# Optimization experiments

Measured on AMD Instinct MI355X. Metric: run time of the kernel, lower is better.

The kernel has to match this reference:

```python
import jax, jax.numpy as jnp
import numpy as np

SEQLS = [256, 256, 256, 256]
HEADS = 8
DIM_HEAD = 64
DIM = 512
SCALE = DIM_HEAD ** -0.5
EPS = 1e-5
# static segment-id per token position: [N]
SEG = np.repeat(np.arange(len(SEQLS)), SEQLS)


def setup_inputs() -> dict:
    key = jax.random.key(0)
    k_x, k_m, k_qkv, k_out = jax.random.split(key, 4)
    B, N = 8, sum(SEQLS)
    inner = HEADS * DIM_HEAD
    x = jax.random.normal(k_x, (B, N, DIM), dtype=jnp.float32)
    m_labels = jax.random.randint(k_m, (B, len(SEQLS)), 0, 2)
    gamma = jnp.ones((DIM,), jnp.float32)
    beta = jnp.zeros((DIM,), jnp.float32)
    w_qkv = jax.random.normal(k_qkv, (DIM, 3 * inner), jnp.float32) * (DIM ** -0.5)
    w_out = jax.random.normal(k_out, (inner, DIM), jnp.float32) * (inner ** -0.5)
    b_out = jnp.zeros((DIM,), jnp.float32)
    return {"x": x, "m_labels": m_labels, "gamma": gamma, "beta": beta,
            "w_qkv": w_qkv, "w_out": w_out, "b_out": b_out}


def reference(x, m_labels, gamma, beta, w_qkv, w_out, b_out):
    B, N, _ = x.shape
    # LayerNorm
    mu = jnp.mean(x, axis=-1, keepdims=True)
    var = jnp.var(x, axis=-1, keepdims=True)
    h = (x - mu) * jax.lax.rsqrt(var + EPS) * gamma + beta
    # QKV projection (no bias)
    qkv = h @ w_qkv  # [B, N, 3*inner]
    q, k, v = jnp.split(qkv, 3, axis=-1)
    to_heads = lambda t: t.reshape(B, N, HEADS, DIM_HEAD).transpose(0, 2, 1, 3)
    q, k, v = to_heads(q), to_heads(k), to_heads(v)  # [B, H, N, D]
    dots = jnp.einsum('bhid,bhjd->bhij', q, k) * SCALE  # [B, H, N, N]
    # modality-block additive mask: -inf on any row/col of a missing modality
    missing = (m_labels == 0)[:, SEG]  # [B, N]
    blocked = missing[:, :, None] | missing[:, None, :]  # [B, N, N]
    dots = jnp.where(blocked[:, None, :, :], -jnp.inf, dots)
    # custom softmax: rows that are fully -inf output 0
    all_inf = jnp.all(jnp.isinf(dots), axis=-1, keepdims=True)
    safe = jnp.where(all_inf, 0.0, dots)
    attn = jax.nn.softmax(safe, axis=-1)
    attn = jnp.where(all_inf, 0.0, attn)
    out = jnp.einsum('bhij,bhjd->bhid', attn, v)  # [B, H, N, D]
    out = out.transpose(0, 2, 1, 3).reshape(B, N, HEADS * DIM_HEAD)
    return out @ w_out + b_out
```

## Files before the change

kernel.cpp:

```cpp
#include <hip/hip_runtime.h>

typedef _Float16 f16;
typedef _Float16 f16x8 __attribute__((ext_vector_type(8)));
typedef float f32x4 __attribute__((ext_vector_type(4)));

typedef __attribute__((address_space(1))) void gvoid;
typedef __attribute__((address_space(3))) void lvoid;
#define GLD16(gp, lp) __builtin_amdgcn_global_load_lds((gvoid*)(gp), (lvoid*)(lp), 16, 0, 0)

__device__ __forceinline__ f32x4 mfma16(f16x8 a, f16x8 b, f32x4 c) {
    return __builtin_amdgcn_mfma_f32_16x16x32_f16(a, b, c, 0, 0, 0);
}

__global__ __launch_bounds__(256) void k_prep(
    const float* __restrict__ x, const float* __restrict__ gamma,
    const float* __restrict__ beta, const int* __restrict__ mlab,
    const float* __restrict__ wqkv, const float* __restrict__ wout,
    f16* __restrict__ h, f16* __restrict__ wqkvT, f16* __restrict__ woutT)
{
    __shared__ float t[64][65];
    int bid = blockIdx.x, tid = threadIdx.x;
    if (bid < 2048) {
        int row = bid * 4 + (tid >> 6);
        int b = row >> 10, seg = (row >> 8) & 3;
        if (mlab[b * 4 + seg] == 0) return;
        int lane = tid & 63;
        const float* xr = x + (size_t)row * 512;
        float4 a = ((const float4*)xr)[lane * 2];
        float4 bv = ((const float4*)xr)[lane * 2 + 1];
        float v[8] = {a.x, a.y, a.z, a.w, bv.x, bv.y, bv.z, bv.w};
        float s = 0.f, s2 = 0.f;
#pragma unroll
        for (int j = 0; j < 8; ++j) { s += v[j]; s2 += v[j] * v[j]; }
#pragma unroll
        for (int off = 1; off < 64; off <<= 1) {
            s  += __shfl_xor(s, off);
            s2 += __shfl_xor(s2, off);
        }
        float mu  = s * (1.f / 512.f);
        float var = s2 * (1.f / 512.f) - mu * mu;
        float rstd = rsqrtf(var + 1e-5f);
        float4 g0 = ((const float4*)gamma)[lane * 2];
        float4 g1 = ((const float4*)gamma)[lane * 2 + 1];
        float4 b0 = ((const float4*)beta)[lane * 2];
        float4 b1 = ((const float4*)beta)[lane * 2 + 1];
        float g[8]  = {g0.x, g0.y, g0.z, g0.w, g1.x, g1.y, g1.z, g1.w};
        float bb[8] = {b0.x, b0.y, b0.z, b0.w, b1.x, b1.y, b1.z, b1.w};
        f16x8 o;
#pragma unroll
        for (int j = 0; j < 8; ++j) o[j] = (f16)((v[j] - mu) * rstd * g[j] + bb[j]);
        *(f16x8*)&h[(size_t)row * 512 + lane * 8] = o;
        return;
    }
    const float* in; f16* out; int C, c0, r0;
    if (bid < 2240) { int idx = bid - 2048; in = wqkv; out = wqkvT; C = 1536; c0 = (idx % 24) * 64; r0 = (idx / 24) * 64; }
    else            { int idx = bid - 2240; in = wout; out = woutT; C = 512;  c0 = (idx % 8)  * 64; r0 = (idx / 8)  * 64; }
#pragma unroll
    for (int i = 0; i < 16; ++i) {
        int r = i * 4 + (tid >> 6), c = tid & 63;
        t[r][c] = in[(size_t)(r0 + r) * C + c0 + c];
    }
    __syncthreads();
#pragma unroll
    for (int i = 0; i < 16; ++i) {
        int cr = i * 4 + (tid >> 6), cc = tid & 63;
        out[(size_t)(c0 + cr) * 512 + r0 + cc] = (f16)t[cc][cr];
    }
}

__global__ __launch_bounds__(256, 3) void k_gemm_qkv(
    const f16* __restrict__ A, const f16* __restrict__ Bt, const int* __restrict__ mlab,
    f16* __restrict__ q, f16* __restrict__ kmat, f16* __restrict__ vt)
{
    __shared__ f16 As[2][64 * 64];
    __shared__ f16 Bs[2][128 * 64];
    int tid = threadIdx.x, wid = tid >> 6, lane = tid & 63;
    int wm = wid >> 1, wn = wid & 1;
    int l15 = lane & 15, l4 = lane >> 4;
    int rowBase = blockIdx.y * 64;
    int colBase = blockIdx.x * 128;
    if (mlab[(rowBase >> 10) * 4 + ((rowBase & 1023) >> 8)] == 0) return;

    int srow = lane >> 3;
    int scolz = ((lane & 7) ^ srow) << 3;
    int kxor = (l15 & 7) << 3;

#define STG(bi, kt)                                                                         \
    do {                                                                                    \
        _Pragma("unroll") for (int i_ = 0; i_ < 2; ++i_) {                                  \
            int rg = (wid * 2 + i_) * 8;                                                    \
            GLD16(&A[(size_t)(rowBase + rg + srow) * 512 + (kt) + scolz], &As[bi][rg * 64]);\
        }                                                                                   \
        _Pragma("unroll") for (int i_ = 0; i_ < 4; ++i_) {                                  \
            int rg = (wid * 4 + i_) * 8;                                                    \
            GLD16(&Bt[(size_t)(colBase + rg + srow) * 512 + (kt) + scolz], &Bs[bi][rg * 64]);\
        }                                                                                   \
    } while (0)

    f32x4 acc[2][4] = {};
    STG(0, 0);
    for (int ki = 0; ki < 8; ++ki) {
        int bi = ki & 1;
        __syncthreads();
        if (ki < 7) STG(bi ^ 1, (ki + 1) * 64);
#pragma unroll
        for (int kk = 0; kk < 2; ++kk) {
            f16x8 af[2], bf[4];
#pragma unroll
            for (int m = 0; m < 2; ++m)
                af[m] = *(const f16x8*)&As[bi][(wm * 32 + m * 16 + l15) * 64 + ((kk * 32 + l4 * 8) ^ kxor)];
#pragma unroll
            for (int n = 0; n < 4; ++n)
                bf[n] = *(const f16x8*)&Bs[bi][(wn * 64 + n * 16 + l15) * 64 + ((kk * 32 + l4 * 8) ^ kxor)];
#pragma unroll
            for (int m = 0; m < 2; ++m)
#pragma unroll
                for (int n = 0; n < 4; ++n)
                    acc[m][n] = mfma16(af[m], bf[n], acc[m][n]);
        }
    }
#undef STG
#pragma unroll
    for (int m = 0; m < 2; ++m)
#pragma unroll
        for (int n = 0; n < 4; ++n)
#pragma unroll
            for (int r = 0; r < 4; ++r) {
                int row = rowBase + wm * 32 + m * 16 + l4 * 4 + r;
                int col = colBase + wn * 64 + n * 16 + l15;
                f16 hv = (f16)acc[m][n][r];
                int b = row >> 10, nt = row & 1023;
                int which = col >> 9, hh = (col >> 6) & 7, d = col & 63;
                size_t hidx = ((size_t)(b * 8 + hh) * 1024 + nt) * 64 + d;
                if (which == 0)      q[hidx] = hv;
                else if (which == 1) kmat[hidx] = hv;
                else                 vt[((size_t)(b * 8 + hh) * 64 + d) * 1024 + nt] = hv;
            }
}

__global__ __launch_bounds__(256, 5) void k_attn(
    const f16* __restrict__ q, const f16* __restrict__ kmat,
    const f16* __restrict__ vt, const int* __restrict__ mlab,
    f16* __restrict__ ao)
{
    __shared__ f16 Ks[2][64 * 64];
    __shared__ f16 Vs[2][64 * 64];

    int bid = blockIdx.x;
    int bh = (bid & 7) + 8 * (bid >> 7);
    int qb = (bid >> 3) & 15;
    int b = bh >> 3, hh = bh & 7;
    int tid = threadIdx.x, wid = tid >> 6, lane = tid & 63;
    int l15 = lane & 15, l4 = lane >> 4;
    int qbase = qb * 64;
    size_t bhs = (size_t)bh;

    if (mlab[b * 4 + (qb >> 2)] == 0) return;

    unsigned long long chpack = 0; int nch = 0;
#pragma unroll
    for (int s = 0; s < 4; ++s)
        if (mlab[b * 4 + s] != 0) {
#pragma unroll
            for (int j = 0; j < 4; ++j) {
                chpack |= (unsigned long long)(4 * s + j) << (4 * nch);
                ++nch;
            }
        }

    f16x8 qf[2];
#pragma unroll
    for (int kk = 0; kk < 2; ++kk) {
        qf[kk] = *(const f16x8*)&q[(bhs * 1024 + qbase + wid * 16 + l15) * 64 + kk * 32 + l4 * 8];
#pragma unroll
        for (int j = 0; j < 8; ++j) qf[kk][j] = qf[kk][j] * (f16)0.125;
    }

    int srow0 = tid >> 3;
    int sc0 = ((tid & 7) ^ (srow0 & 7)) << 3;
    int srow1 = (tid + 256) >> 3;
    int sc1 = (((tid + 256) & 7) ^ (srow1 & 7)) << 3;
    int ldsbase0 = (wid * 64) * 8;
    int ldsbase1 = (wid * 64 + 256) * 8;

#define STAGE(bi, t0)                                                                   \
    do {                                                                                \
        GLD16(&kmat[(bhs * 1024 + (t0) + srow0) * 64 + sc0], &Ks[bi][ldsbase0]);        \
        GLD16(&kmat[(bhs * 1024 + (t0) + srow1) * 64 + sc1], &Ks[bi][ldsbase1]);        \
        GLD16(&vt[(bhs * 64 + srow0) * 1024 + (t0) + sc0],   &Vs[bi][ldsbase0]);        \
        GLD16(&vt[(bhs * 64 + srow1) * 1024 + (t0) + sc1],   &Vs[bi][ldsbase1]);        \
    } while (0)

    float mrun = -1e30f, lrun = 0.f;
    f32x4 o[4] = {};
    int kxor = (l15 & 7) << 3;
    int srcA = l15 + ((l4 & 1) * 2) * 16;
    int srcB = srcA + 16;
    int sel = l4 >> 1;

    STAGE(0, (int)(chpack & 15) << 6);

    for (int c = 0; c < nch; ++c) {
        int bi = c & 1;
        __syncthreads();
        if (c + 1 < nch) {
            int t0n = (int)((chpack >> (4 * (c + 1))) & 15) << 6;
            STAGE(bi ^ 1, t0n);
        }

        f32x4 st[4] = {};
#pragma unroll
        for (int kk = 0; kk < 2; ++kk)
#pragma unroll
            for (int n = 0; n < 4; ++n) {
                f16x8 ka = *(const f16x8*)&Ks[bi][(n * 16 + l15) * 64 + ((kk * 32 + l4 * 8) ^ kxor)];
                st[n] = mfma16(ka, qf[kk], st[n]);
            }

        f32x4 m4 = st[0];
#pragma unroll
        for (int n = 1; n < 4; ++n)
#pragma unroll
            for (int r = 0; r < 4; ++r) m4[r] = fmaxf(m4[r], st[n][r]);
        float mx = fmaxf(fmaxf(m4[0], m4[1]), fmaxf(m4[2], m4[3]));
        mx = fmaxf(mx, __shfl_xor(mx, 16));
        mx = fmaxf(mx, __shfl_xor(mx, 32));
        float mnew = fmaxf(mrun, mx);
        float alpha = __expf(mrun - mnew);
        mrun = mnew;
        float rs = 0.f;
        union PK { f16 h[4]; long long ll; } pk[4];
#pragma unroll
        for (int n = 0; n < 4; ++n)
#pragma unroll
            for (int r = 0; r < 4; ++r) {
                float p = __expf(st[n][r] - mnew);
                rs += p;
                pk[n].h[r] = (f16)p;
            }
        rs += __shfl_xor(rs, 16);
        rs += __shfl_xor(rs, 32);
        lrun = lrun * alpha + rs;
#pragma unroll
        for (int nd = 0; nd < 4; ++nd) o[nd] *= alpha;

#pragma unroll
        for (int ks = 0; ks < 2; ++ks) {
            long long A0 = __shfl(pk[ks * 2].ll,     srcA);
            long long A1 = __shfl(pk[ks * 2 + 1].ll, srcA);
            long long B0 = __shfl(pk[ks * 2].ll,     srcB);
            long long B1 = __shfl(pk[ks * 2 + 1].ll, srcB);
            union PB { long long ll[2]; f16x8 v; } pb;
            pb.ll[0] = sel ? A1 : A0;
            pb.ll[1] = sel ? B1 : B0;
#pragma unroll
            for (int nd = 0; nd < 4; ++nd) {
                f16x8 va = *(const f16x8*)&Vs[bi][(nd * 16 + l15) * 64 + ((ks * 32 + l4 * 8) ^ kxor)];
                o[nd] = mfma16(va, pb.v, o[nd]);
            }
        }
    }
#undef STAGE

    float inv = 1.f / lrun;
    int qrow = qbase + wid * 16 + l15;
#pragma unroll
    for (int nd = 0; nd < 4; ++nd) {
        union { f16 h[4]; long long ll; } w;
#pragma unroll
        for (int r = 0; r < 4; ++r) w.h[r] = (f16)(o[nd][r] * inv);
        *(long long*)&ao[(size_t)(b * 1024 + qrow) * 512 + hh * 64 + nd * 16 + l4 * 4] = w.ll;
    }
}

__global__ __launch_bounds__(256, 3) void k_gemm_out(
    const f16* __restrict__ A, const f16* __restrict__ Bt, const int* __restrict__ mlab,
    const float* __restrict__ bias, float* __restrict__ out)
{
    __shared__ f16 As[2][64 * 64];
    __shared__ f16 Bs[2][128 * 64];
    int tid = threadIdx.x, wid = tid >> 6, lane = tid & 63;
    int wm = wid >> 1, wn = wid & 1;
    int l15 = lane & 15, l4 = lane >> 4;
    int rowBase = blockIdx.y * 64;
    int colBase = blockIdx.x * 128;
    if (mlab[(rowBase >> 10) * 4 + ((rowBase & 1023) >> 8)] == 0) {
        for (int i = tid; i < 64 * 128; i += 256)
            out[(size_t)(rowBase + (i >> 7)) * 512 + colBase + (i & 127)] = bias[colBase + (i & 127)];
        return;
    }

    int srow = lane >> 3;
    int scolz = ((lane & 7) ^ srow) << 3;
    int kxor = (l15 & 7) << 3;

#define STG(bi, kt)                                                                         \
    do {                                                                                    \
        _Pragma("unroll") for (int i_ = 0; i_ < 2; ++i_) {                                  \
            int rg = (wid * 2 + i_) * 8;                                                    \
            GLD16(&A[(size_t)(rowBase + rg + srow) * 512 + (kt) + scolz], &As[bi][rg * 64]);\
        }                                                                                   \
        _Pragma("unroll") for (int i_ = 0; i_ < 4; ++i_) {                                  \
            int rg = (wid * 4 + i_) * 8;                                                    \
            GLD16(&Bt[(size_t)(colBase + rg + srow) * 512 + (kt) + scolz], &Bs[bi][rg * 64]);\
        }                                                                                   \
    } while (0)

    f32x4 acc[2][4] = {};
    STG(0, 0);
    for (int ki = 0; ki < 8; ++ki) {
        int bi = ki & 1;
        __syncthreads();
        if (ki < 7) STG(bi ^ 1, (ki + 1) * 64);
#pragma unroll
        for (int kk = 0; kk < 2; ++kk) {
            f16x8 af[2], bf[4];
#pragma unroll
            for (int m = 0; m < 2; ++m)
                af[m] = *(const f16x8*)&As[bi][(wm * 32 + m * 16 + l15) * 64 + ((kk * 32 + l4 * 8) ^ kxor)];
#pragma unroll
            for (int n = 0; n < 4; ++n)
                bf[n] = *(const f16x8*)&Bs[bi][(wn * 64 + n * 16 + l15) * 64 + ((kk * 32 + l4 * 8) ^ kxor)];
#pragma unroll
            for (int m = 0; m < 2; ++m)
#pragma unroll
                for (int n = 0; n < 4; ++n)
                    acc[m][n] = mfma16(af[m], bf[n], acc[m][n]);
        }
    }
#undef STG
#pragma unroll
    for (int m = 0; m < 2; ++m)
#pragma unroll
        for (int n = 0; n < 4; ++n)
#pragma unroll
            for (int r = 0; r < 4; ++r) {
                int row = rowBase + wm * 32 + m * 16 + l4 * 4 + r;
                int col = colBase + wn * 64 + n * 16 + l15;
                out[(size_t)row * 512 + col] = acc[m][n][r] + bias[col];
            }
}

extern "C" void kernel_launch(void* const* d_in, const int* in_sizes, int n_in,
                              void* d_out, int out_size, void* d_ws, size_t ws_size,
                              hipStream_t stream) {
    const float* x     = (const float*)d_in[0];
    const int*   mlab  = (const int*)d_in[1];
    const float* gamma = (const float*)d_in[2];
    const float* beta  = (const float*)d_in[3];
    const float* wqkv  = (const float*)d_in[4];
    const float* wout  = (const float*)d_in[5];
    const float* bout  = (const float*)d_in[6];
    float* out = (float*)d_out;

    f16* h     = (f16*)d_ws;
    f16* wqkvT = h + 8192 * 512;
    f16* woutT = wqkvT + 1536 * 512;
    f16* q     = woutT + 512 * 512;
    f16* kmat  = q + 4 * 1024 * 1024;
    f16* vt    = kmat + 4 * 1024 * 1024;
    f16* ao    = h;

    k_prep<<<2304, 256, 0, stream>>>(x, gamma, beta, mlab, wqkv, wout, h, wqkvT, woutT);
    k_gemm_qkv<<<dim3(12, 128), 256, 0, stream>>>(h, wqkvT, mlab, q, kmat, vt);
    k_attn<<<1024, 256, 0, stream>>>(q, kmat, vt, mlab, ao);
    k_gemm_out<<<dim3(4, 128), 256, 0, stream>>>(ao, woutT, mlab, bout, out);
}
```

Baseline: 73.67 us.

## Split attention KV chunks across two wave groups with LDS merge

```diff
diff --git a/kernel.cpp b/kernel.cpp
--- a/kernel.cpp
+++ b/kernel.cpp
@@ -138,19 +138,20 @@
             }
 }
 
-__global__ __launch_bounds__(256, 5) void k_attn(
+__global__ __launch_bounds__(512, 4) void k_attn(
     const f16* __restrict__ q, const f16* __restrict__ kmat,
     const f16* __restrict__ vt, const int* __restrict__ mlab,
     f16* __restrict__ ao)
 {
-    __shared__ f16 Ks[2][64 * 64];
-    __shared__ f16 Vs[2][64 * 64];
+    __shared__ f16 Ks[2][2][64 * 64];
+    __shared__ f16 Vs[2][2][64 * 64];
 
     int bid = blockIdx.x;
     int bh = (bid & 7) + 8 * (bid >> 7);
     int qb = (bid >> 3) & 15;
     int b = bh >> 3, hh = bh & 7;
     int tid = threadIdx.x, wid = tid >> 6, lane = tid & 63;
+    int qs = wid & 3, g = wid >> 2;
     int l15 = lane & 15, l4 = lane >> 4;
     int qbase = qb * 64;
     size_t bhs = (size_t)bh;
@@ -167,28 +168,31 @@
                 ++nch;
             }
         }
+    int niter = nch >> 1;
 
     f16x8 qf[2];
 #pragma unroll
     for (int kk = 0; kk < 2; ++kk) {
-        qf[kk] = *(const f16x8*)&q[(bhs * 1024 + qbase + wid * 16 + l15) * 64 + kk * 32 + l4 * 8];
+        qf[kk] = *(const f16x8*)&q[(bhs * 1024 + qbase + qs * 16 + l15) * 64 + kk * 32 + l4 * 8];
 #pragma unroll
         for (int j = 0; j < 8; ++j) qf[kk][j] = qf[kk][j] * (f16)0.125;
     }
 
-    int srow0 = tid >> 3;
-    int sc0 = ((tid & 7) ^ (srow0 & 7)) << 3;
-    int srow1 = (tid + 256) >> 3;
-    int sc1 = (((tid + 256) & 7) ^ (srow1 & 7)) << 3;
-    int ldsbase0 = (wid * 64) * 8;
-    int ldsbase1 = (wid * 64 + 256) * 8;
+    int gtid = tid & 255;
+    int gw = wid & 3;
+    int srow0 = gtid >> 3;
+    int sc0 = ((gtid & 7) ^ (srow0 & 7)) << 3;
+    int srow1 = (gtid + 256) >> 3;
+    int sc1 = (((gtid + 256) & 7) ^ (srow1 & 7)) << 3;
+    int lb0 = (gw * 64) * 8;
+    int lb1 = (gw * 64 + 256) * 8;
 
 #define STAGE(bi, t0)                                                                   \
     do {                                                                                \
-        GLD16(&kmat[(bhs * 1024 + (t0) + srow0) * 64 + sc0], &Ks[bi][ldsbase0]);        \
-        GLD16(&kmat[(bhs * 1024 + (t0) + srow1) * 64 + sc1], &Ks[bi][ldsbase1]);        \
-        GLD16(&vt[(bhs * 64 + srow0) * 1024 + (t0) + sc0],   &Vs[bi][ldsbase0]);        \
-        GLD16(&vt[(bhs * 64 + srow1) * 1024 + (t0) + sc1],   &Vs[bi][ldsbase1]);        \
+        GLD16(&kmat[(bhs * 1024 + (t0) + srow0) * 64 + sc0], &Ks[g][bi][lb0]);          \
+        GLD16(&kmat[(bhs * 1024 + (t0) + srow1) * 64 + sc1], &Ks[g][bi][lb1]);          \
+        GLD16(&vt[(bhs * 64 + srow0) * 1024 + (t0) + sc0],   &Vs[g][bi][lb0]);          \
+        GLD16(&vt[(bhs * 64 + srow1) * 1024 + (t0) + sc1],   &Vs[g][bi][lb1]);          \
     } while (0)
 
     float mrun = -1e30f, lrun = 0.f;
@@ -198,24 +202,27 @@
     int srcB = srcA + 16;
     int sel = l4 >> 1;
 
-    STAGE(0, (int)(chpack & 15) << 6);
-
-    for (int c = 0; c < nch; ++c) {
-        int bi = c & 1;
+    STAGE(0, (int)((chpack >> (4 * g)) & 15) << 6);
+
+    for (int i = 0; i < niter; ++i) {
+        int bi = i & 1;
         __syncthreads();
-        if (c + 1 < nch) {
-            int t0n = (int)((chpack >> (4 * (c + 1))) & 15) << 6;
+        if (i + 1 < niter) {
+            int cn = 2 * (i + 1) + g;
+            int t0n = (int)((chpack >> (4 * cn)) & 15) << 6;
             STAGE(bi ^ 1, t0n);
         }
 
         f32x4 st[4] = {};
+        __builtin_amdgcn_s_setprio(1);
 #pragma unroll
         for (int kk = 0; kk < 2; ++kk)
 #pragma unroll
             for (int n = 0; n < 4; ++n) {
-                f16x8 ka = *(const f16x8*)&Ks[bi][(n * 16 + l15) * 64 + ((kk * 32 + l4 * 8) ^ kxor)];
+                f16x8 ka = *(const f16x8*)&Ks[g][bi][(n * 16 + l15) * 64 + ((kk * 32 + l4 * 8) ^ kxor)];
                 st[n] = mfma16(ka, qf[kk], st[n]);
             }
+        __builtin_amdgcn_s_setprio(0);
 
         f32x4 m4 = st[0];
 #pragma unroll
@@ -253,23 +260,43 @@
             union PB { long long ll[2]; f16x8 v; } pb;
             pb.ll[0] = sel ? A1 : A0;
             pb.ll[1] = sel ? B1 : B0;
+            __builtin_amdgcn_s_setprio(1);
 #pragma unroll
             for (int nd = 0; nd < 4; ++nd) {
-                f16x8 va = *(const f16x8*)&Vs[bi][(nd * 16 + l15) * 64 + ((ks * 32 + l4 * 8) ^ kxor)];
+                f16x8 va = *(const f16x8*)&Vs[g][bi][(nd * 16 + l15) * 64 + ((ks * 32 + l4 * 8) ^ kxor)];
                 o[nd] = mfma16(va, pb.v, o[nd]);
             }
+            __builtin_amdgcn_s_setprio(0);
         }
     }
 #undef STAGE
 
-    float inv = 1.f / lrun;
-    int qrow = qbase + wid * 16 + l15;
-#pragma unroll
-    for (int nd = 0; nd < 4; ++nd) {
-        union { f16 h[4]; long long ll; } w;
-#pragma unroll
-        for (int r = 0; r < 4; ++r) w.h[r] = (f16)(o[nd][r] * inv);
-        *(long long*)&ao[(size_t)(b * 1024 + qrow) * 512 + hh * 64 + nd * 16 + l4 * 4] = w.ll;
+    float* mg  = (float*)&Ks[0][0][0];
+    float* mml = (float*)&Vs[0][0][0];
+    __syncthreads();
+    if (g == 1) {
+        if (l4 == 0) { mml[qs * 16 + l15] = mrun; mml[64 + qs * 16 + l15] = lrun; }
+#pragma unroll
+        for (int nd = 0; nd < 4; ++nd)
+#pragma unroll
+            for (int r = 0; r < 4; ++r)
+                mg[(qs * 64 + nd * 16 + l4 * 4 + r) * 16 + l15] = o[nd][r];
+    }
+    __syncthreads();
+    if (g == 0) {
+        float m1 = mml[qs * 16 + l15], l1 = mml[64 + qs * 16 + l15];
+        float mst = fmaxf(mrun, m1);
+        float e0 = __expf(mrun - mst), e1 = __expf(m1 - mst);
+        float inv = 1.f / (lrun * e0 + l1 * e1);
+        int qrow = qbase + qs * 16 + l15;
+#pragma unroll
+        for (int nd = 0; nd < 4; ++nd) {
+            union { f16 h[4]; long long ll; } w;
+#pragma unroll
+            for (int r = 0; r < 4; ++r)
+                w.h[r] = (f16)((o[nd][r] * e0 + mg[(qs * 64 + nd * 16 + l4 * 4 + r) * 16 + l15] * e1) * inv);
+            *(long long*)&ao[(size_t)(b * 1024 + qrow) * 512 + hh * 64 + nd * 16 + l4 * 4] = w.ll;
+        }
     }
 }
 
@@ -363,6 +390,6 @@
 
     k_prep<<<2304, 256, 0, stream>>>(x, gamma, beta, mlab, wqkv, wout, h, wqkvT, woutT);
     k_gemm_qkv<<<dim3(12, 128), 256, 0, stream>>>(h, wqkvT, mlab, q, kmat, vt);
-    k_attn<<<1024, 256, 0, stream>>>(q, kmat, vt, mlab, ao);
+    k_attn<<<1024, 512, 0, stream>>>(q, kmat, vt, mlab, ao);
     k_gemm_out<<<dim3(4, 128), 256, 0, stream>>>(ao, woutT, mlab, bout, out);
 }
```

Measured after the change: 68.93 us. -6.4%, faster.
